# Optimization experiments

Measured on AMD Instinct MI355X. Metric: run time of the kernel, lower is better.

The kernel has to match this reference:

```python
import jax, jax.numpy as jnp
import numpy as np

H = 8    # heads
DH = 64  # dim_head


def _attn(q, k, v):
    sim = jnp.einsum('bid,bjd->bij', q, k)
    a = jax.nn.softmax(sim, axis=-1)
    return jnp.einsum('bij,bjd->bid', a, v)


def setup_inputs() -> dict:
    key = jax.random.key(0)
    k1, k2, k3 = jax.random.split(key, 3)
    B, f, n, dim = 8, 16, 196, 512
    N = 1 + f * n  # cls token + f*n patch tokens
    x = jax.random.normal(k1, (B, N, dim), jnp.float32)
    W_qkv = jax.random.normal(k2, (dim, 3 * H * DH), jnp.float32) * 0.02
    W_out = jax.random.normal(k3, (H * DH, dim), jnp.float32) * 0.02
    b_out = jnp.zeros((dim,), jnp.float32)
    return {"x": x, "W_qkv": W_qkv, "W_out": W_out, "b_out": b_out, "f": f, "n": n}


def reference(x, W_qkv, W_out, b_out, f, n):
    B, N, dim = x.shape
    scale = DH ** -0.5
    qkv = x @ W_qkv                                   # [B, N, 3*H*DH]
    q, k, v = jnp.split(qkv, 3, axis=-1)
    # 'b n (h d) -> (b h) n d'
    to_bh = lambda t: t.reshape(B, N, H, DH).transpose(0, 2, 1, 3).reshape(B * H, N, DH)
    q, k, v = map(to_bh, (q, k, v))
    q = q * scale
    cls_q, q_ = q[:, :1], q[:, 1:]
    cls_k, k_ = k[:, :1], k[:, 1:]
    cls_v, v_ = v[:, :1], v[:, 1:]
    # cls token attends to everything
    cls_out = _attn(cls_q, k, v)                      # [B*H, 1, DH]
    # 'b (f n) d -> (b n) f d'
    to_time = lambda t: t.reshape(B * H, f, n, DH).transpose(0, 2, 1, 3).reshape(B * H * n, f, DH)
    q_, k_, v_ = map(to_time, (q_, k_, v_))
    # repeat cls k/v to each spatial location: 'b () d -> (b r) () d', r = n
    rep = lambda t: jnp.broadcast_to(t[:, None], (B * H, n, 1, DH)).reshape(B * H * n, 1, DH)
    k_ = jnp.concatenate([rep(cls_k), k_], axis=1)    # [B*H*n, f+1, DH]
    v_ = jnp.concatenate([rep(cls_v), v_], axis=1)
    out = _attn(q_, k_, v_)                           # [B*H*n, f, DH]
    # '(b n) f d -> b (f n) d'
    out = out.reshape(B * H, n, f, DH).transpose(0, 2, 1, 3).reshape(B * H, f * n, DH)
    out = jnp.concatenate([cls_out, out], axis=1)     # [B*H, N, DH]
    # '(b h) n d -> b n (h d)'
    out = out.reshape(B, H, N, DH).transpose(0, 2, 1, 3).reshape(B, N, H * DH)
    return out @ W_out + b_out
```

## Files before the change

kernel.cpp:

```cpp
#include <hip/hip_runtime.h>
#include <hip/hip_bf16.h>

#define B_    8
#define H_    8
#define DH_   64
#define FR    16
#define SP    196
#define NTOK  3137
#define DIM   512
#define NQKV  1536
#define MREAL (B_ * NTOK)
#define MPAD  25216

#define CSPLIT 50
#define CTOK   64

typedef __bf16 bf16x8 __attribute__((ext_vector_type(8)));
typedef float  f32x4  __attribute__((ext_vector_type(4)));
typedef unsigned short ushort8 __attribute__((ext_vector_type(8)));

__device__ __forceinline__ float bf2f(unsigned short u) {
    union { unsigned int i; float f; } x; x.i = ((unsigned int)u) << 16; return x.f;
}
__device__ __forceinline__ unsigned short f2bf(float f) {
    __hip_bfloat16 h = __float2bfloat16(f);
    union { __hip_bfloat16 h; unsigned short u; } x; x.h = h; return x.u;
}


__global__ __launch_bounds__(256) void convert_pad_x(const float* __restrict__ x,
                                                     unsigned short* __restrict__ xb) {
    int idx = blockIdx.x * 256 + threadIdx.x;
    const int real8 = MREAL * DIM / 8;
    ushort8 o;
    if (idx < real8) {
        f32x4 a = *(const f32x4*)(x + (size_t)idx * 8);
        f32x4 b = *(const f32x4*)(x + (size_t)idx * 8 + 4);
        o[0] = f2bf(a[0]); o[1] = f2bf(a[1]); o[2] = f2bf(a[2]); o[3] = f2bf(a[3]);
        o[4] = f2bf(b[0]); o[5] = f2bf(b[1]); o[6] = f2bf(b[2]); o[7] = f2bf(b[3]);
    } else {
        o = (ushort8){0,0,0,0,0,0,0,0};
    }
    *(ushort8*)(xb + (size_t)idx * 8) = o;
}

__global__ __launch_bounds__(256) void transpose_w(const float* __restrict__ W,
                                                   unsigned short* __restrict__ WT,
                                                   int K, int Nn) {
    __shared__ float tile[32][33];
    int n0 = blockIdx.x * 32, k0 = blockIdx.y * 32;
    int tx = threadIdx.x & 31, ty = threadIdx.x >> 5;
#pragma unroll
    for (int r = 0; r < 32; r += 8)
        tile[ty + r][tx] = W[(size_t)(k0 + ty + r) * Nn + n0 + tx];
    __syncthreads();
#pragma unroll
    for (int r = 0; r < 32; r += 8)
        WT[(size_t)(n0 + ty + r) * K + k0 + tx] = f2bf(tile[tx][ty + r]);
}

__global__ __launch_bounds__(256) void zero_pad_attn(unsigned short* __restrict__ attn) {
    int idx = blockIdx.x * 256 + threadIdx.x;
    ushort8 z = (ushort8){0,0,0,0,0,0,0,0};
    *(ushort8*)(attn + (size_t)MREAL * DIM + (size_t)idx * 8) = z;
}


__device__ __forceinline__ void gload_lds16(const unsigned short* g, unsigned short* l) {
    __builtin_amdgcn_global_load_lds((const __attribute__((address_space(1))) void*)g,
                                     (__attribute__((address_space(3))) void*)l, 16, 0, 0);
}

#define PATCH_M 16

template<int EPI>
__global__ __launch_bounds__(256)
void gemm_bt(const unsigned short* __restrict__ A, const unsigned short* __restrict__ Bt,
             unsigned short* __restrict__ Cb, float* __restrict__ Cf,
             const float* __restrict__ bias, int Nn, int K, int nM, int nN) {
    __shared__ __attribute__((aligned(16))) unsigned short As[2][128 * 32];
    __shared__ __attribute__((aligned(16))) unsigned short Bs[2][128 * 32];

    int id = blockIdx.x;
    int pid = id / (PATCH_M * nN);
    int rem = id - pid * (PATCH_M * nN);
    int m0 = pid * PATCH_M;
    int pm = min(PATCH_M, nM - m0);
    int tM = m0 + (rem % pm);
    int tN = rem / pm;

    int wave = threadIdx.x >> 6, lane = threadIdx.x & 63;
    int wm = wave >> 1, wn = wave & 1;
    const int r15 = lane & 15, kq = (lane >> 4) * 8;
    f32x4 acc[4][4] = {};

    const unsigned short* Abase = A  + (size_t)(tM * 128) * K;
    const unsigned short* Bbase = Bt + (size_t)(tN * 128) * K;

    const int ce0 = wave * 64 + lane;
    const int ce1 = ce0 + 256;

#define STAGE(buf, k0)                                                          \
    {                                                                           \
        _Pragma("unroll")                                                       \
        for (int r = 0; r < 2; ++r) {                                           \
            int chunk = (r * 4 + wave) * 64;                                    \
            int ce = chunk + lane;                                              \
            int row = ce >> 2, kp = (ce & 3) * 8;                               \
            gload_lds16(Abase + (size_t)row * K + (k0) + kp, &As[buf][chunk * 8]); \
            gload_lds16(Bbase + (size_t)row * K + (k0) + kp, &Bs[buf][chunk * 8]); \
        }                                                                       \
    }

    STAGE(0, 0)
    asm volatile("s_waitcnt vmcnt(0)" ::: "memory");
    __builtin_amdgcn_s_barrier();

    const int nK = K / 32;
    int cur = 0;
    for (int kt = 0; kt < nK; ++kt) {
        if (kt + 1 < nK) STAGE(cur ^ 1, (kt + 1) * 32)
        bf16x8 af[4], bg[4];
#pragma unroll
        for (int m = 0; m < 4; m++)
            af[m] = *(const bf16x8*)&As[cur][(wm * 64 + m * 16 + r15) * 32 + kq];
#pragma unroll
        for (int nn2 = 0; nn2 < 4; nn2++)
            bg[nn2] = *(const bf16x8*)&Bs[cur][(wn * 64 + nn2 * 16 + r15) * 32 + kq];
        __builtin_amdgcn_s_setprio(1);
#pragma unroll
        for (int m = 0; m < 4; m++)
#pragma unroll
            for (int nn2 = 0; nn2 < 4; nn2++)
                acc[m][nn2] = __builtin_amdgcn_mfma_f32_16x16x32_bf16(af[m], bg[nn2], acc[m][nn2], 0, 0, 0);
        __builtin_amdgcn_s_setprio(0);
        asm volatile("s_waitcnt vmcnt(0)" ::: "memory");
        __builtin_amdgcn_s_barrier();
        cur ^= 1;
    }
#undef STAGE

    int rowBase = tM * 128 + wm * 64 + (lane >> 4) * 4;
    int colBase = tN * 128 + wn * 64 + r15;
#pragma unroll
    for (int m = 0; m < 4; m++) {
#pragma unroll
        for (int nn2 = 0; nn2 < 4; nn2++) {
            int col = colBase + nn2 * 16;
#pragma unroll
            for (int i = 0; i < 4; i++) {
                int row = rowBase + m * 16 + i;
                float v = acc[m][nn2][i];
                if constexpr (EPI == 0) {
                    if (col < DIM) v *= 0.125f;
                    Cb[(size_t)row * Nn + col] = f2bf(v);
                } else {
                    if (row < MREAL) Cf[(size_t)row * Nn + col] = v + bias[col];
                }
            }
        }
    }
}

__global__ __launch_bounds__(256) void cls_partial(const unsigned short* __restrict__ qkv,
                                                   float* __restrict__ part) {
    int bh = blockIdx.y, split = blockIdx.x;
    int b = bh >> 3, h = bh & 7;
    int tid = threadIdx.x;
    size_t base = (size_t)b * NTOK * NQKV + h * 64;
    int t0 = split * CTOK;

    __shared__ float qls[64];
    __shared__ float sim[CTOK];
    __shared__ __attribute__((aligned(16))) unsigned short Vs[CTOK][64];
    __shared__ float red[256];
    __shared__ float Ms, Ss;

    if (tid < 64) qls[tid] = bf2f(qkv[base + tid]);

    {
        int t = tid >> 2, q = tid & 3;
        size_t g = base + (size_t)(t0 + t) * NQKV + 1024 + q * 16;
        *(ushort8*)&Vs[t][q * 16]     = *(const ushort8*)(qkv + g);
        *(ushort8*)&Vs[t][q * 16 + 8] = *(const ushort8*)(qkv + g + 8);
    }
    __syncthreads();

    float pacc = 0.f;
    {
        int t = tid >> 2, q = tid & 3;
        size_t g = base + (size_t)(t0 + t) * NQKV + 512 + q * 16;
        bf16x8 k0 = *(const bf16x8*)(qkv + g);
        bf16x8 k1 = *(const bf16x8*)(qkv + g + 8);
#pragma unroll
        for (int e = 0; e < 8; e++) {
            pacc += qls[q * 16 + e]     * (float)k0[e];
            pacc += qls[q * 16 + 8 + e] * (float)k1[e];
        }
    }
    pacc += __shfl_xor(pacc, 1);
    pacc += __shfl_xor(pacc, 2);
    if ((tid & 3) == 0) {
        int t = tid >> 2;
        sim[t] = (t0 + t < NTOK) ? pacc : -1e30f;
    }
    __syncthreads();

    if (tid < 64) {
        float m = sim[tid];
#pragma unroll
        for (int off = 32; off > 0; off >>= 1) m = fmaxf(m, __shfl_xor(m, off));
        float p = __expf(sim[tid] - m);
        sim[tid] = p;
        float s = p;
#pragma unroll
        for (int off = 32; off > 0; off >>= 1) s += __shfl_xor(s, off);
        if (tid == 0) { Ms = m; Ss = s; }
    }
    __syncthreads();

    int d = tid & 63, grp = tid >> 6;
    float acc = 0.f;
#pragma unroll
    for (int t = grp * 16; t < grp * 16 + 16; t++)
        acc += sim[t] * bf2f(Vs[t][d]);
    red[tid] = acc; __syncthreads();
    if (tid < 64) {
        float pv = red[tid] + red[tid + 64] + red[tid + 128] + red[tid + 192];
        float* pp = part + ((size_t)bh * CSPLIT + split) * 66;
        pp[2 + tid] = pv;
        if (tid == 0) { pp[0] = Ms; pp[1] = Ss; }
    }
}

__global__ __launch_bounds__(64) void cls_reduce(const float* __restrict__ part,
                                                 unsigned short* __restrict__ attn) {
    int bh = blockIdx.x, b = bh >> 3, h = bh & 7;
    int d = threadIdx.x;
    const float* pp = part + (size_t)bh * CSPLIT * 66;
    float M = -1e30f;
    for (int i = 0; i < CSPLIT; i++) M = fmaxf(M, pp[i * 66]);
    float S = 0.f, PV = 0.f;
    for (int i = 0; i < CSPLIT; i++) {
        float w = __expf(pp[i * 66] - M);
        S  += pp[i * 66 + 1] * w;
        PV += pp[i * 66 + 2 + d] * w;
    }
    attn[(size_t)(b * NTOK) * DIM + h * 64 + d] = f2bf(PV / S);
}

__global__ __launch_bounds__(256) void time_attn(const unsigned short* __restrict__ qkv,
                                                 unsigned short* __restrict__ attn) {
    int wave = threadIdx.x >> 6, lane = threadIdx.x & 63;
    int seq = blockIdx.x * 4 + wave;
    int bh = seq / SP, s = seq % SP;
    int b = bh >> 3, h = bh & 7;
    __shared__ __attribute__((aligned(16))) unsigned short Q[4][16][72];
    __shared__ __attribute__((aligned(16))) unsigned short Kt[4][17][72];
    __shared__ __attribute__((aligned(16))) unsigned short Vt[4][17][72];
    __shared__ float S[4][16][18];
    size_t base = (size_t)b * NTOK * NQKV + h * 64;

#pragma unroll
    for (int c = lane; c < 128; c += 64) {
        int i = c >> 3, part = c & 7;
        size_t g = base + (size_t)(1 + i * SP + s) * NQKV + part * 8;
        *(ushort8*)&Q[wave][i][part * 8] = *(const ushort8*)(qkv + g);
    }
    for (int c = lane; c < 136; c += 64) {
        int j = c >> 3, part = c & 7;
        int t = (j == 0) ? 0 : (1 + (j - 1) * SP + s);
        size_t g = base + (size_t)t * NQKV + part * 8;
        *(ushort8*)&Kt[wave][j][part * 8] = *(const ushort8*)(qkv + g + 512);
        *(ushort8*)&Vt[wave][j][part * 8] = *(const ushort8*)(qkv + g + 1024);
    }
    __syncthreads();

    for (int p = lane; p < 272; p += 64) {
        int i = p / 17, j = p - i * 17;
        float acc = 0.f;
#pragma unroll
        for (int c = 0; c < 8; c++) {
            bf16x8 qv = *(const bf16x8*)&Q[wave][i][c * 8];
            bf16x8 kv = *(const bf16x8*)&Kt[wave][j][c * 8];
#pragma unroll
            for (int e = 0; e < 8; e++) acc += (float)qv[e] * (float)kv[e];
        }
        S[wave][i][j] = acc;
    }
    __syncthreads();

    if (lane < 16) {
        int i = lane;
        float m = -1e30f;
#pragma unroll
        for (int j = 0; j < 17; j++) m = fmaxf(m, S[wave][i][j]);
        float sum = 0.f;
#pragma unroll
        for (int j = 0; j < 17; j++) {
            float p = __expf(S[wave][i][j] - m);
            S[wave][i][j] = p; sum += p;
        }
        float invs = 1.f / sum;
#pragma unroll
        for (int j = 0; j < 17; j++) S[wave][i][j] *= invs;
    }
    __syncthreads();

#pragma unroll
    for (int i = 0; i < 16; i++) {
        float acc = 0.f;
#pragma unroll
        for (int j = 0; j < 17; j++)
            acc += S[wave][i][j] * bf2f(Vt[wave][j][lane]);
        attn[(size_t)(b * NTOK + 1 + i * SP + s) * DIM + h * 64 + lane] = f2bf(acc);
    }
}


extern "C" void kernel_launch(void* const* d_in, const int* in_sizes, int n_in,
                              void* d_out, int out_size, void* d_ws, size_t ws_size,
                              hipStream_t stream) {
    (void)in_sizes; (void)n_in; (void)out_size; (void)ws_size;
    const float* x    = (const float*)d_in[0];
    const float* Wqkv = (const float*)d_in[1];
    const float* Wout = (const float*)d_in[2];
    const float* bout = (const float*)d_in[3];
    float* out = (float*)d_out;

    unsigned short* xb    = (unsigned short*)d_ws;
    unsigned short* qkv   = xb    + (size_t)MPAD * DIM;
    unsigned short* attn  = qkv   + (size_t)MPAD * NQKV;
    unsigned short* wqkvT = attn  + (size_t)MPAD * DIM;
    unsigned short* woutT = wqkvT + (size_t)NQKV * DIM;
    float* clspart = (float*)xb;

    convert_pad_x<<<MPAD * DIM / 8 / 256, 256, 0, stream>>>(x, xb);
    transpose_w<<<dim3(NQKV / 32, DIM / 32), 256, 0, stream>>>(Wqkv, wqkvT, DIM, NQKV);
    transpose_w<<<dim3(DIM / 32, DIM / 32), 256, 0, stream>>>(Wout, woutT, DIM, DIM);
    zero_pad_attn<<<(MPAD - MREAL) * DIM / 8 / 256, 256, 0, stream>>>(attn);

    const int nM = MPAD / 128;
    gemm_bt<0><<<nM * (NQKV / 128), 256, 0, stream>>>(
        xb, wqkvT, qkv, nullptr, nullptr, NQKV, DIM, nM, NQKV / 128);

    cls_partial<<<dim3(CSPLIT, B_ * H_), 256, 0, stream>>>(qkv, clspart);
    cls_reduce<<<B_ * H_, 64, 0, stream>>>(clspart, attn);
    time_attn<<<(B_ * H_ * SP) / 4, 256, 0, stream>>>(qkv, attn);

    gemm_bt<1><<<nM * (DIM / 128), 256, 0, stream>>>(
        attn, woutT, nullptr, out, bout, DIM, DIM, nM, DIM / 128);
}
```

Baseline: 298.6 us.

## Use MFMA for time-attention QK^T and PV with transposed V in LDS

Rewrites the per-sequence time attention kernel to compute QK^T and P·V with bf16 16x16x32 MFMA instructions instead of scalar dot products. V is stored transposed in LDS with zero padding, and the softmax runs in registers using cross-lane shuffles instead of a single 16-lane loop over shared memory. This aims to remove scalar FMA work and the serial softmax. The trade-offs are a transposed scalar LDS store of V, rounding the probabilities to bf16, and wasted MFMA columns on the 17-wide padding.

```diff
diff --git a/kernel.cpp b/kernel.cpp
--- a/kernel.cpp
+++ b/kernel.cpp
@@ -97,9 +97,6 @@
     const unsigned short* Abase = A  + (size_t)(tM * 128) * K;
     const unsigned short* Bbase = Bt + (size_t)(tN * 128) * K;
 
-    const int ce0 = wave * 64 + lane;
-    const int ce1 = ce0 + 256;
-
 #define STAGE(buf, k0)                                                          \
     {                                                                           \
         _Pragma("unroll")                                                       \
@@ -249,72 +246,101 @@
     attn[(size_t)(b * NTOK) * DIM + h * 64 + d] = f2bf(PV / S);
 }
 
+#define QOFF 0
+#define KOFF 1408
+#define VOFF 2904
+#define POFF 5464
+#define WSLICE 6112
+
 __global__ __launch_bounds__(256) void time_attn(const unsigned short* __restrict__ qkv,
                                                  unsigned short* __restrict__ attn) {
+    __shared__ __attribute__((aligned(16))) unsigned short lds[4][WSLICE];
     int wave = threadIdx.x >> 6, lane = threadIdx.x & 63;
+    unsigned short* W = lds[wave];
     int seq = blockIdx.x * 4 + wave;
-    int bh = seq / SP, s = seq % SP;
+    int bh = seq / SP, s = seq - bh * SP;
     int b = bh >> 3, h = bh & 7;
-    __shared__ __attribute__((aligned(16))) unsigned short Q[4][16][72];
-    __shared__ __attribute__((aligned(16))) unsigned short Kt[4][17][72];
-    __shared__ __attribute__((aligned(16))) unsigned short Vt[4][17][72];
-    __shared__ float S[4][16][18];
     size_t base = (size_t)b * NTOK * NQKV + h * 64;
-
-#pragma unroll
-    for (int c = lane; c < 128; c += 64) {
+    const int r15 = lane & 15, q4 = lane >> 4, kq = q4 * 8;
+
+    {
+        ushort8 z = (ushort8){0,0,0,0,0,0,0,0};
+#pragma unroll
+        for (int r = 0; r < 2; ++r) {
+            int c = r * 64 + lane;
+            *(ushort8*)&W[VOFF + (c >> 1) * 40 + 16 + (c & 1) * 8] = z;
+        }
+    }
+#pragma unroll
+    for (int r = 0; r < 2; ++r) {
+        int c = r * 64 + lane;
         int i = c >> 3, part = c & 7;
-        size_t g = base + (size_t)(1 + i * SP + s) * NQKV + part * 8;
-        *(ushort8*)&Q[wave][i][part * 8] = *(const ushort8*)(qkv + g);
+        *(ushort8*)&W[QOFF + i * 88 + part * 8] =
+            *(const ushort8*)(qkv + base + (size_t)(1 + i * SP + s) * NQKV + part * 8);
     }
     for (int c = lane; c < 136; c += 64) {
         int j = c >> 3, part = c & 7;
         int t = (j == 0) ? 0 : (1 + (j - 1) * SP + s);
-        size_t g = base + (size_t)t * NQKV + part * 8;
-        *(ushort8*)&Kt[wave][j][part * 8] = *(const ushort8*)(qkv + g + 512);
-        *(ushort8*)&Vt[wave][j][part * 8] = *(const ushort8*)(qkv + g + 1024);
-    }
-    __syncthreads();
-
-    for (int p = lane; p < 272; p += 64) {
-        int i = p / 17, j = p - i * 17;
-        float acc = 0.f;
-#pragma unroll
-        for (int c = 0; c < 8; c++) {
-            bf16x8 qv = *(const bf16x8*)&Q[wave][i][c * 8];
-            bf16x8 kv = *(const bf16x8*)&Kt[wave][j][c * 8];
-#pragma unroll
-            for (int e = 0; e < 8; e++) acc += (float)qv[e] * (float)kv[e];
+        const unsigned short* g = qkv + base + (size_t)t * NQKV + part * 8;
+        *(ushort8*)&W[KOFF + j * 88 + part * 8] = *(const ushort8*)(g + 512);
+        ushort8 v = *(const ushort8*)(g + 1024);
+#pragma unroll
+        for (int e = 0; e < 8; e++)
+            W[VOFF + (part * 8 + e) * 40 + j] = v[e];
+    }
+    __syncthreads();
+
+    f32x4 sc0 = {0.f, 0.f, 0.f, 0.f}, sc1 = {0.f, 0.f, 0.f, 0.f};
+#pragma unroll
+    for (int ks = 0; ks < 2; ++ks) {
+        bf16x8 aq = *(const bf16x8*)&W[QOFF + r15 * 88 + ks * 32 + kq];
+        bf16x8 b0 = *(const bf16x8*)&W[KOFF + r15 * 88 + ks * 32 + kq];
+        bf16x8 b1 = *(const bf16x8*)&W[KOFF + (16 + r15) * 88 + ks * 32 + kq];
+        sc0 = __builtin_amdgcn_mfma_f32_16x16x32_bf16(aq, b0, sc0, 0, 0, 0);
+        sc1 = __builtin_amdgcn_mfma_f32_16x16x32_bf16(aq, b1, sc1, 0, 0, 0);
+    }
+
+#pragma unroll
+    for (int i = 0; i < 4; ++i) {
+        float t0 = sc0[i];
+        float t1 = sc1[i];
+        float t1v = (r15 == 0) ? t1 : -1e30f;
+        float m = fmaxf(t0, t1v);
+        m = fmaxf(m, __shfl_xor(m, 1));
+        m = fmaxf(m, __shfl_xor(m, 2));
+        m = fmaxf(m, __shfl_xor(m, 4));
+        m = fmaxf(m, __shfl_xor(m, 8));
+        float p0 = __expf(t0 - m);
+        float p1 = (r15 == 0) ? __expf(t1 - m) : 0.f;
+        float sum = p0 + p1;
+        sum += __shfl_xor(sum, 1);
+        sum += __shfl_xor(sum, 2);
+        sum += __shfl_xor(sum, 4);
+        sum += __shfl_xor(sum, 8);
+        float inv = 1.f / sum;
+        int f = q4 * 4 + i;
+        W[POFF + f * 40 + r15]      = f2bf(p0 * inv);
+        W[POFF + f * 40 + 16 + r15] = f2bf(p1 * inv);
+    }
+    __syncthreads();
+
+    bf16x8 ap = *(const bf16x8*)&W[POFF + r15 * 40 + kq];
+    f32x4 o[4];
+#pragma unroll
+    for (int t = 0; t < 4; ++t) {
+        f32x4 z = {0.f, 0.f, 0.f, 0.f};
+        bf16x8 bv = *(const bf16x8*)&W[VOFF + (t * 16 + r15) * 40 + kq];
+        o[t] = __builtin_amdgcn_mfma_f32_16x16x32_bf16(ap, bv, z, 0, 0, 0);
+    }
+
+#pragma unroll
+    for (int t = 0; t < 4; ++t)
+#pragma unroll
+        for (int i = 0; i < 4; ++i) {
+            int f = q4 * 4 + i;
+            attn[(size_t)(b * NTOK + 1 + f * SP + s) * DIM + h * 64 + t * 16 + r15] =
+                f2bf(o[t][i]);
         }
-        S[wave][i][j] = acc;
-    }
-    __syncthreads();
-
-    if (lane < 16) {
-        int i = lane;
-        float m = -1e30f;
-#pragma unroll
-        for (int j = 0; j < 17; j++) m = fmaxf(m, S[wave][i][j]);
-        float sum = 0.f;
-#pragma unroll
-        for (int j = 0; j < 17; j++) {
-            float p = __expf(S[wave][i][j] - m);
-            S[wave][i][j] = p; sum += p;
-        }
-        float invs = 1.f / sum;
-#pragma unroll
-        for (int j = 0; j < 17; j++) S[wave][i][j] *= invs;
-    }
-    __syncthreads();
-
-#pragma unroll
-    for (int i = 0; i < 16; i++) {
-        float acc = 0.f;
-#pragma unroll
-        for (int j = 0; j < 17; j++)
-            acc += S[wave][i][j] * bf2f(Vt[wave][j][lane]);
-        attn[(size_t)(b * NTOK + 1 + i * SP + s) * DIM + h * 64 + lane] = f2bf(acc);
-    }
 }
 
 
```

After: 259.8 us. -13.0%, faster.
